# Kernel tuning notes

Measured on AMD Instinct MI355X. Metric: run time of the kernel, lower is better.

The kernel has to match this reference:

```python
import jax, jax.numpy as jnp
import numpy as np

SEQ_LEN = 12      # PRED_LEN
H_DIM = 128
EMB_DIM = 64
NPEDS = 65536


def setup_inputs() -> dict:
    key = jax.random.key(0)
    ks = jax.random.split(key, 12)
    s = 0.05
    return {
        "last_pos": jax.random.normal(ks[0], (NPEDS, 2), jnp.float32),
        "last_pos_rel": jax.random.normal(ks[1], (NPEDS, 2), jnp.float32),
        "h0": jax.random.normal(ks[2], (NPEDS, H_DIM), jnp.float32),
        "c0": jax.random.normal(ks[3], (NPEDS, H_DIM), jnp.float32),
        # LSTM params (torch gate order: i, f, g, o)
        "w_ih": jax.random.normal(ks[4], (4 * H_DIM, EMB_DIM), jnp.float32) * s,
        "w_hh": jax.random.normal(ks[5], (4 * H_DIM, H_DIM), jnp.float32) * s,
        "b_ih": jax.random.normal(ks[6], (4 * H_DIM,), jnp.float32) * s,
        "b_hh": jax.random.normal(ks[7], (4 * H_DIM,), jnp.float32) * s,
        # spatial_embedding: Linear(2, EMB_DIM)
        "w_se": jax.random.normal(ks[8], (EMB_DIM, 2), jnp.float32) * s,
        "b_se": jax.random.normal(ks[9], (EMB_DIM,), jnp.float32) * s,
        # hidden2pos: Linear(H_DIM, 2)
        "w_hp": jax.random.normal(ks[10], (2, H_DIM), jnp.float32) * s,
        "b_hp": jax.random.normal(ks[11], (2,), jnp.float32) * s,
    }


def reference(last_pos, last_pos_rel, h0, c0,
              w_ih, w_hh, b_ih, b_hh, w_se, b_se, w_hp, b_hp):
    b = b_ih + b_hh  # fold the two LSTM biases
    dec_in0 = last_pos_rel @ w_se.T + b_se          # [N, EMB]

    def step(carry, _):
        h, c, dec_in, lp = carry
        gates = dec_in @ w_ih.T + h @ w_hh.T + b    # [N, 4H]
        i, f, g, o = jnp.split(gates, 4, axis=-1)
        c = jax.nn.sigmoid(f) * c + jax.nn.sigmoid(i) * jnp.tanh(g)
        h = jax.nn.sigmoid(o) * jnp.tanh(c)
        rel = h @ w_hp.T + b_hp                     # [N, 2]
        lp = rel + lp                               # curr_pos
        dec_in = rel @ w_se.T + b_se                # next embedding input
        return (h, c, dec_in, lp), rel

    _, rels = jax.lax.scan(step, (h0, c0, dec_in0, last_pos), None, length=SEQ_LEN)
    return rels  # [SEQ_LEN, N, 2] == pred_traj_fake_rel
```

## Files before the change

### kernel.cpp

```cpp
#include <hip/hip_runtime.h>
#include <hip/hip_bf16.h>

typedef __attribute__((ext_vector_type(8))) short bf16x8;
typedef __attribute__((ext_vector_type(4))) short bf16x4;
typedef __attribute__((ext_vector_type(4))) float f32x4;

#define NPEDS 65536
#define SEQ 12
#define HD 128
#define ED 64
#define MBLK 64
#define P1 136
#define WHH_FRAGS 128
#define WEFF_FRAGS 132
#define NFRAGS (WHH_FRAGS + WEFF_FRAGS)
#define L2E 1.44269504088896340736f
#define NEG2L (-2.88539008177792681472f)

__device__ __forceinline__ short f2bf(float x) {
  __hip_bfloat16 b = __float2bfloat16(x);
  return __builtin_bit_cast(short, b);
}
__device__ __forceinline__ float exp2_(float x) {
#if __has_builtin(__builtin_amdgcn_exp2f)
  return __builtin_amdgcn_exp2f(x);
#else
  return exp2f(x);
#endif
}

__device__ __forceinline__ int pe_grp(int a) {
  return (a >> 3) * 32 + (a & 3) * 8 + ((a >> 2) & 1) * 4;
}

__global__ void prep_kernel(const float* __restrict__ w_ih,
                            const float* __restrict__ w_hh,
                            const float* __restrict__ w_se,
                            const float* __restrict__ w_hp,
                            const float* __restrict__ b_ih,
                            const float* __restrict__ b_hh,
                            const float* __restrict__ b_se,
                            const float* __restrict__ b_hp,
                            short* __restrict__ wsB, float* __restrict__ fl) {
  int t = blockIdx.x * 256 + threadIdx.x;
  if (t < WHH_FRAGS * 64) {
    int frag = t >> 6, l = t & 63;
    int cc = frag >> 4, g = (frag >> 2) & 3, kt = frag & 3;
    float fac = (g == 2) ? 2.0f * L2E : L2E;
    int n = g * HD + cc * 16 + (l & 15);
    bf16x8 v;
#pragma unroll
    for (int e = 0; e < 8; ++e) {
      int k = kt * 32 + ((l >> 4) << 2) + (e & 3) + ((e >> 2) << 4);
      v[e] = f2bf(w_hh[n * HD + k] * fac);
    }
    *(bf16x8*)(wsB + (size_t)frag * 512 + l * 8) = v;
  } else if (t < NFRAGS * 64) {
    int u = t - WHH_FRAGS * 64;
    int frag = u >> 6, l = u & 63;
    int llo = l & 15;
    int ks[8];
#pragma unroll
    for (int e = 0; e < 8; ++e)
      ks[e] = (frag & 3) * 32 + ((l >> 4) << 2) + (e & 3) + ((e >> 2) << 4);
    float acc[8];
    if (frag < 128) {
      int cc = frag >> 4, g = (frag >> 2) & 3;
      float fac = (g == 2) ? 2.0f * L2E : L2E;
      int n = g * HD + cc * 16 + llo;
#pragma unroll
      for (int e = 0; e < 8; ++e) acc[e] = w_hh[n * HD + ks[e]];
      for (int j = 0; j < ED; ++j) {
        float wij = w_ih[n * ED + j];
        float se0 = w_se[2 * j], se1 = w_se[2 * j + 1];
#pragma unroll
        for (int e = 0; e < 8; ++e)
          acc[e] += wij * (se0 * w_hp[ks[e]] + se1 * w_hp[HD + ks[e]]);
      }
#pragma unroll
      for (int e = 0; e < 8; ++e) acc[e] *= fac;
    } else {
#pragma unroll
      for (int e = 0; e < 8; ++e)
        acc[e] = (llo < 2) ? w_hp[llo * HD + ks[e]] : 0.f;
    }
    bf16x8 v;
#pragma unroll
    for (int e = 0; e < 8; ++e) v[e] = f2bf(acc[e]);
    *(bf16x8*)(wsB + (size_t)(WHH_FRAGS + frag) * 512 + l * 8) = v;
  } else if (t < NFRAGS * 64 + 512) {
    int n = t - NFRAGS * 64;
    float fac = ((n >> 7) == 2) ? 2.0f * L2E : L2E;
    float b = b_ih[n] + b_hh[n];
    float s0 = 0.f, w20 = 0.f, w21 = 0.f;
    for (int j = 0; j < ED; ++j) {
      float wij = w_ih[n * ED + j];
      s0 += wij * b_se[j];
      w20 += wij * w_se[2 * j];
      w21 += wij * w_se[2 * j + 1];
    }
    fl[n] = fac * (b + s0 + w20 * b_hp[0] + w21 * b_hp[1]);
    fl[512 + n] = fac * (b + s0);
    fl[1024 + 2 * n] = fac * w20;
    fl[1024 + 2 * n + 1] = fac * w21;
  }
}

__global__ __launch_bounds__(512, 4) void lstm_kernel(
    const float* __restrict__ lpr, const float* __restrict__ h0,
    const float* __restrict__ c0, const float* __restrict__ b_hp,
    const short* __restrict__ wsB, const float* __restrict__ fl,
    float* __restrict__ out) {
  __shared__ __align__(16) short hb[2][MBLK * P1];
  __shared__ __align__(16) short s_wsR[4 * 512];
  __shared__ float s_beff[512];
  __shared__ float s_lpr[MBLK * 2];

  const int tid = threadIdx.x;
  const int cc = tid >> 6;
  const int l = tid & 63;
  const int lhi = l >> 4;
  const int llo = l & 15;
  const int p0 = blockIdx.x * MBLK;
  const int hoff = (cc >> 1) * 32 + (llo >> 2) * 8 + (cc & 1) * 4 + (llo & 3);

  if (tid < 128) s_lpr[tid] = lpr[(size_t)p0 * 2 + tid];
  s_beff[tid] = fl[tid];
  ((unsigned long long*)s_wsR)[tid] =
      ((const unsigned long long*)(wsB + (size_t)(WHH_FRAGS + 128) * 512))[tid];

  bf16x8 Bw[4][4];
#pragma unroll
  for (int g = 0; g < 4; ++g)
#pragma unroll
    for (int kt = 0; kt < 4; ++kt)
      Bw[g][kt] = *(const bf16x8*)(wsB +
                      (size_t)((cc * 4 + g) * 4 + kt) * 512 + l * 8);

  float creg[4][4];
#pragma unroll
  for (int Mt = 0; Mt < 4; ++Mt)
#pragma unroll
    for (int r = 0; r < 4; ++r)
      creg[Mt][r] =
          c0[(size_t)(p0 + Mt * 16 + lhi * 4 + r) * HD + cc * 16 + llo];

  const float bhp_l = (llo < 2) ? b_hp[llo] : 0.f;

#pragma unroll
  for (int i = 0; i < 4; ++i) {
    int grp = i * 512 + tid;
    int p = grp >> 5, a = grp & 31;
    f32x4 v = *(const f32x4*)(h0 + (size_t)(p0 + p) * HD + a * 4);
    bf16x4 s;
    s[0] = f2bf(v[0]); s[1] = f2bf(v[1]); s[2] = f2bf(v[2]); s[3] = f2bf(v[3]);
    *(bf16x4*)(&hb[0][p * P1 + pe_grp(a)]) = s;
  }
  __syncthreads();

  auto update_mt = [&](f32x4 (&acc)[4], float (&cr)[4], int rowb, short* An) {
#pragma unroll
    for (int r = 0; r < 4; ++r) {
      float yi = acc[0][r], yf = acc[1][r];
      float yg = acc[2][r], yo = acc[3][r];
      float P = 1.f + exp2_(-yf);
      float Q = 1.f + exp2_(-yi);
      float R = 1.f + exp2_(-yg);
      float QR = Q * R;
      float rD = __builtin_amdgcn_rcpf(P * QR);
      float cn = (cr[r] * QR + (2.f - R) * P) * rD;
      cr[r] = cn;
      float T = 1.f + exp2_(cn * NEG2L);
      float S = 1.f + exp2_(-yo);
      float hn = (2.f - T) * __builtin_amdgcn_rcpf(S * T);
      An[(rowb + r) * P1 + hoff] = f2bf(hn);
    }
  };

  {
    float b0r[4], w20r[4], w21r[4];
#pragma unroll
    for (int g = 0; g < 4; ++g) {
      int n = g * HD + cc * 16 + llo;
      b0r[g] = fl[512 + n];
      w20r[g] = fl[1024 + 2 * n];
      w21r[g] = fl[1024 + 2 * n + 1];
    }
#pragma unroll
    for (int Mt = 0; Mt < 4; ++Mt) {
      bf16x8 Af[4];
#pragma unroll
      for (int kt = 0; kt < 4; ++kt)
        Af[kt] =
            *(const bf16x8*)(&hb[0][(Mt * 16 + llo) * P1 + kt * 32 + lhi * 8]);
      f32x4 acc[4];
#pragma unroll
      for (int g = 0; g < 4; ++g)
#pragma unroll
        for (int r = 0; r < 4; ++r) {
          int row = Mt * 16 + lhi * 4 + r;
          acc[g][r] =
              b0r[g] + w20r[g] * s_lpr[row * 2] + w21r[g] * s_lpr[row * 2 + 1];
        }
#pragma unroll
      for (int kt = 0; kt < 4; ++kt)
#pragma unroll
        for (int g = 0; g < 4; ++g)
          acc[g] = __builtin_amdgcn_mfma_f32_16x16x32_bf16(Af[kt], Bw[g][kt],
                                                           acc[g], 0, 0, 0);
      update_mt(acc, creg[Mt], Mt * 16 + lhi * 4, hb[1]);
    }
    __syncthreads();
  }

  const short* wsW = wsB + (size_t)WHH_FRAGS * 512;
#pragma unroll
  for (int g = 0; g < 4; ++g)
#pragma unroll
    for (int kt = 0; kt < 4; ++kt)
      Bw[g][kt] = *(const bf16x8*)(wsW +
                      (size_t)((cc * 4 + g) * 4 + kt) * 512 + l * 8);

  const int relMt = cc - 4;
  for (int s = 1; s < SEQ; ++s) {
    const short* A = hb[s & 1];
    short* An = hb[(s + 1) & 1];
    f32x4 ar = {bhp_l, bhp_l, bhp_l, bhp_l};
#pragma unroll
    for (int Mt = 0; Mt < 4; ++Mt) {
      bf16x8 Af[4];
#pragma unroll
      for (int kt = 0; kt < 4; ++kt)
        Af[kt] =
            *(const bf16x8*)(&A[(Mt * 16 + llo) * P1 + kt * 32 + lhi * 8]);
      f32x4 acc[4];
#pragma unroll
      for (int g = 0; g < 4; ++g) {
        float b = s_beff[g * HD + cc * 16 + llo];
        acc[g] = {b, b, b, b};
      }
#pragma unroll
      for (int kt = 0; kt < 4; ++kt)
#pragma unroll
        for (int g = 0; g < 4; ++g)
          acc[g] = __builtin_amdgcn_mfma_f32_16x16x32_bf16(Af[kt], Bw[g][kt],
                                                           acc[g], 0, 0, 0);
      if (cc >= 4 && Mt == relMt) {
#pragma unroll
        for (int kt = 0; kt < 4; ++kt) {
          bf16x8 BfR = *(const bf16x8*)(s_wsR + kt * 512 + l * 8);
          ar = __builtin_amdgcn_mfma_f32_16x16x32_bf16(Af[kt], BfR, ar, 0, 0,
                                                       0);
        }
      }
      update_mt(acc, creg[Mt], Mt * 16 + lhi * 4, An);
    }
    if (cc >= 4 && llo < 2) {
#pragma unroll
      for (int r = 0; r < 4; ++r)
        out[(size_t)(s - 1) * (NPEDS * 2) +
            (size_t)(p0 + relMt * 16 + lhi * 4 + r) * 2 + llo] = ar[r];
    }
    __syncthreads();
  }

  if (cc >= 4) {
    const short* A = hb[SEQ & 1];
    f32x4 ar = {bhp_l, bhp_l, bhp_l, bhp_l};
#pragma unroll
    for (int kt = 0; kt < 4; ++kt) {
      bf16x8 BfR = *(const bf16x8*)(s_wsR + kt * 512 + l * 8);
      bf16x8 Afr =
          *(const bf16x8*)(&A[(relMt * 16 + llo) * P1 + kt * 32 + lhi * 8]);
      ar = __builtin_amdgcn_mfma_f32_16x16x32_bf16(Afr, BfR, ar, 0, 0, 0);
    }
    if (llo < 2) {
#pragma unroll
      for (int r = 0; r < 4; ++r)
        out[(size_t)(SEQ - 1) * (NPEDS * 2) +
            (size_t)(p0 + relMt * 16 + lhi * 4 + r) * 2 + llo] = ar[r];
    }
  }
}

extern "C" void kernel_launch(void* const* d_in, const int* in_sizes, int n_in,
                              void* d_out, int out_size, void* d_ws,
                              size_t ws_size, hipStream_t stream) {
  const float* lpr = (const float*)d_in[1];
  const float* h0 = (const float*)d_in[2];
  const float* c0 = (const float*)d_in[3];
  const float* w_ih = (const float*)d_in[4];
  const float* w_hh = (const float*)d_in[5];
  const float* b_ih = (const float*)d_in[6];
  const float* b_hh = (const float*)d_in[7];
  const float* w_se = (const float*)d_in[8];
  const float* b_se = (const float*)d_in[9];
  const float* w_hp = (const float*)d_in[10];
  const float* b_hp = (const float*)d_in[11];
  short* wsB = (short*)d_ws;
  float* fl = (float*)((char*)d_ws + (size_t)NFRAGS * 512 * sizeof(short));
  float* out = (float*)d_out;

  prep_kernel<<<67, 256, 0, stream>>>(w_ih, w_hh, w_se, w_hp, b_ih, b_hh,
                                      b_se, b_hp, wsB, fl);
  lstm_kernel<<<NPEDS / MBLK, 512, 0, stream>>>(lpr, h0, c0, b_hp, wsB, fl,
                                                out);
}
```

Before: 186.8 us.

## Swap MFMA operands so weights are A, double pedestrians per block

Transposes the per-step gate GEMM so the weight fragments are the A operand and the hidden state is B. Each lane now holds 4 consecutive hidden units for one pedestrian, which allows vectorized bf16x4 writes of h into a new swizzled LDS layout. The block tile grows from 64 to 128 pedestrians with 8 pedestrian tiles per wave, and launch bounds drop to 2 blocks per CU. Bias and hidden2pos weights move from LDS into registers. All 8 waves now compute rel outputs instead of 4. The cost is higher register pressure from 8 c-state tiles per thread and lower occupancy, in exchange for amortizing weight fragments across more MFMAs and fewer LDS stores.

```diff
diff --git a/kernel.cpp b/kernel.cpp
--- a/kernel.cpp
+++ b/kernel.cpp
@@ -4,13 +4,14 @@
 typedef __attribute__((ext_vector_type(8))) short bf16x8;
 typedef __attribute__((ext_vector_type(4))) short bf16x4;
 typedef __attribute__((ext_vector_type(4))) float f32x4;
+typedef __attribute__((ext_vector_type(2))) float f32x2;
 
 #define NPEDS 65536
 #define SEQ 12
 #define HD 128
 #define ED 64
-#define MBLK 64
-#define P1 136
+#define MBLK 128
+#define NPT 8
 #define WHH_FRAGS 128
 #define WEFF_FRAGS 132
 #define NFRAGS (WHH_FRAGS + WEFF_FRAGS)
@@ -29,8 +30,8 @@
 #endif
 }
 
-__device__ __forceinline__ int pe_grp(int a) {
-  return (a >> 3) * 32 + (a & 3) * 8 + ((a >> 2) & 1) * 4;
+__device__ __forceinline__ int hoff(int Pt, int cg, int lhi, int llo) {
+  return (((Pt * 8 + cg) * 4 + lhi) * 16 + llo) * 4;
 }
 
 __global__ void prep_kernel(const float* __restrict__ w_ih,
@@ -106,15 +107,12 @@
   }
 }
 
-__global__ __launch_bounds__(512, 4) void lstm_kernel(
+__global__ __launch_bounds__(512, 2) void lstm_kernel(
     const float* __restrict__ lpr, const float* __restrict__ h0,
     const float* __restrict__ c0, const float* __restrict__ b_hp,
     const short* __restrict__ wsB, const float* __restrict__ fl,
     float* __restrict__ out) {
-  __shared__ __align__(16) short hb[2][MBLK * P1];
-  __shared__ __align__(16) short s_wsR[4 * 512];
-  __shared__ float s_beff[512];
-  __shared__ float s_lpr[MBLK * 2];
+  __shared__ short hb[2][NPT * 8 * 4 * 16 * 4];
 
   const int tid = threadIdx.x;
   const int cc = tid >> 6;
@@ -122,43 +120,49 @@
   const int lhi = l >> 4;
   const int llo = l & 15;
   const int p0 = blockIdx.x * MBLK;
-  const int hoff = (cc >> 1) * 32 + (llo >> 2) * 8 + (cc & 1) * 4 + (llo & 3);
-
-  if (tid < 128) s_lpr[tid] = lpr[(size_t)p0 * 2 + tid];
-  s_beff[tid] = fl[tid];
-  ((unsigned long long*)s_wsR)[tid] =
-      ((const unsigned long long*)(wsB + (size_t)(WHH_FRAGS + 128) * 512))[tid];
-
-  bf16x8 Bw[4][4];
+
+  bf16x8 Aw[4][4];
 #pragma unroll
   for (int g = 0; g < 4; ++g)
 #pragma unroll
     for (int kt = 0; kt < 4; ++kt)
-      Bw[g][kt] = *(const bf16x8*)(wsB +
+      Aw[g][kt] = *(const bf16x8*)(wsB +
                       (size_t)((cc * 4 + g) * 4 + kt) * 512 + l * 8);
-
-  float creg[4][4];
-#pragma unroll
-  for (int Mt = 0; Mt < 4; ++Mt)
-#pragma unroll
-    for (int r = 0; r < 4; ++r)
-      creg[Mt][r] =
-          c0[(size_t)(p0 + Mt * 16 + lhi * 4 + r) * HD + cc * 16 + llo];
-
-  const float bhp_l = (llo < 2) ? b_hp[llo] : 0.f;
-
-#pragma unroll
-  for (int i = 0; i < 4; ++i) {
-    int grp = i * 512 + tid;
-    int p = grp >> 5, a = grp & 31;
-    f32x4 v = *(const f32x4*)(h0 + (size_t)(p0 + p) * HD + a * 4);
-    bf16x4 s;
-    s[0] = f2bf(v[0]); s[1] = f2bf(v[1]); s[2] = f2bf(v[2]); s[3] = f2bf(v[3]);
-    *(bf16x4*)(&hb[0][p * P1 + pe_grp(a)]) = s;
+  bf16x8 Whp[4];
+#pragma unroll
+  for (int kt = 0; kt < 4; ++kt)
+    Whp[kt] = *(const bf16x8*)(wsB +
+                  (size_t)(WHH_FRAGS + 128 + kt) * 512 + l * 8);
+
+  f32x4 beffv[4];
+#pragma unroll
+  for (int g = 0; g < 4; ++g)
+    beffv[g] = *(const f32x4*)&fl[g * HD + cc * 16 + lhi * 4];
+
+  float creg[NPT][4];
+#pragma unroll
+  for (int Pt = 0; Pt < NPT; ++Pt) {
+    f32x4 cv = *(const f32x4*)&c0[(size_t)(p0 + Pt * 16 + llo) * HD +
+                                  cc * 16 + lhi * 4];
+#pragma unroll
+    for (int r = 0; r < 4; ++r) creg[Pt][r] = cv[r];
+  }
+  const float bhp0 = b_hp[0], bhp1 = b_hp[1];
+
+#pragma unroll
+  for (int i = 0; i < 8; ++i) {
+    int idx = i * 512 + tid;
+    int a = idx & 31, ped = idx >> 5;
+    f32x4 v = *(const f32x4*)&h0[(size_t)(p0 + ped) * HD + a * 4];
+    bf16x4 sv;
+    sv[0] = f2bf(v[0]); sv[1] = f2bf(v[1]);
+    sv[2] = f2bf(v[2]); sv[3] = f2bf(v[3]);
+    *(bf16x4*)&hb[0][hoff(ped >> 4, a >> 2, a & 3, ped & 15)] = sv;
   }
   __syncthreads();
 
-  auto update_mt = [&](f32x4 (&acc)[4], float (&cr)[4], int rowb, short* An) {
+  auto update_pt = [&](f32x4 (&acc)[4], float (&cr)[4], short* An, int Pt) {
+    bf16x4 hn4;
 #pragma unroll
     for (int r = 0; r < 4; ++r) {
       float yi = acc[0][r], yf = acc[1][r];
@@ -172,43 +176,45 @@
       cr[r] = cn;
       float T = 1.f + exp2_(cn * NEG2L);
       float S = 1.f + exp2_(-yo);
-      float hn = (2.f - T) * __builtin_amdgcn_rcpf(S * T);
-      An[(rowb + r) * P1 + hoff] = f2bf(hn);
-    }
+      hn4[r] = f2bf((2.f - T) * __builtin_amdgcn_rcpf(S * T));
+    }
+    *(bf16x4*)&An[hoff(Pt, cc, lhi, llo)] = hn4;
   };
 
   {
-    float b0r[4], w20r[4], w21r[4];
+    f32x4 b0v[4], wa[4], wb[4];
 #pragma unroll
     for (int g = 0; g < 4; ++g) {
-      int n = g * HD + cc * 16 + llo;
-      b0r[g] = fl[512 + n];
-      w20r[g] = fl[1024 + 2 * n];
-      w21r[g] = fl[1024 + 2 * n + 1];
-    }
-#pragma unroll
-    for (int Mt = 0; Mt < 4; ++Mt) {
-      bf16x8 Af[4];
+      int n0 = g * HD + cc * 16 + lhi * 4;
+      b0v[g] = *(const f32x4*)&fl[512 + n0];
+      wa[g] = *(const f32x4*)&fl[1024 + 2 * n0];
+      wb[g] = *(const f32x4*)&fl[1024 + 2 * n0 + 4];
+    }
+#pragma unroll
+    for (int Pt = 0; Pt < NPT; ++Pt) {
+      f32x2 lp = *(const f32x2*)&lpr[(size_t)(p0 + Pt * 16 + llo) * 2];
+      bf16x8 Bh[4];
+#pragma unroll
+      for (int kt = 0; kt < 4; ++kt) {
+        bf16x4 lo = *(const bf16x4*)&hb[0][hoff(Pt, 2 * kt, lhi, llo)];
+        bf16x4 hi = *(const bf16x4*)&hb[0][hoff(Pt, 2 * kt + 1, lhi, llo)];
+        Bh[kt] = __builtin_shufflevector(lo, hi, 0, 1, 2, 3, 4, 5, 6, 7);
+      }
+      f32x4 acc[4];
+#pragma unroll
+      for (int g = 0; g < 4; ++g) {
+        acc[g][0] = b0v[g][0] + wa[g][0] * lp[0] + wa[g][1] * lp[1];
+        acc[g][1] = b0v[g][1] + wa[g][2] * lp[0] + wa[g][3] * lp[1];
+        acc[g][2] = b0v[g][2] + wb[g][0] * lp[0] + wb[g][1] * lp[1];
+        acc[g][3] = b0v[g][3] + wb[g][2] * lp[0] + wb[g][3] * lp[1];
+      }
 #pragma unroll
       for (int kt = 0; kt < 4; ++kt)
-        Af[kt] =
-            *(const bf16x8*)(&hb[0][(Mt * 16 + llo) * P1 + kt * 32 + lhi * 8]);
-      f32x4 acc[4];
-#pragma unroll
-      for (int g = 0; g < 4; ++g)
-#pragma unroll
-        for (int r = 0; r < 4; ++r) {
-          int row = Mt * 16 + lhi * 4 + r;
-          acc[g][r] =
-              b0r[g] + w20r[g] * s_lpr[row * 2] + w21r[g] * s_lpr[row * 2 + 1];
-        }
-#pragma unroll
-      for (int kt = 0; kt < 4; ++kt)
 #pragma unroll
         for (int g = 0; g < 4; ++g)
-          acc[g] = __builtin_amdgcn_mfma_f32_16x16x32_bf16(Af[kt], Bw[g][kt],
+          acc[g] = __builtin_amdgcn_mfma_f32_16x16x32_bf16(Aw[g][kt], Bh[kt],
                                                            acc[g], 0, 0, 0);
-      update_mt(acc, creg[Mt], Mt * 16 + lhi * 4, hb[1]);
+      update_pt(acc, creg[Pt], hb[1], Pt);
     }
     __syncthreads();
   }
@@ -218,67 +224,61 @@
   for (int g = 0; g < 4; ++g)
 #pragma unroll
     for (int kt = 0; kt < 4; ++kt)
-      Bw[g][kt] = *(const bf16x8*)(wsW +
+      Aw[g][kt] = *(const bf16x8*)(wsW +
                       (size_t)((cc * 4 + g) * 4 + kt) * 512 + l * 8);
 
-  const int relMt = cc - 4;
   for (int s = 1; s < SEQ; ++s) {
     const short* A = hb[s & 1];
     short* An = hb[(s + 1) & 1];
-    f32x4 ar = {bhp_l, bhp_l, bhp_l, bhp_l};
-#pragma unroll
-    for (int Mt = 0; Mt < 4; ++Mt) {
-      bf16x8 Af[4];
+#pragma unroll
+    for (int Pt = 0; Pt < NPT; ++Pt) {
+      bf16x8 Bh[4];
+#pragma unroll
+      for (int kt = 0; kt < 4; ++kt) {
+        bf16x4 lo = *(const bf16x4*)&A[hoff(Pt, 2 * kt, lhi, llo)];
+        bf16x4 hi = *(const bf16x4*)&A[hoff(Pt, 2 * kt + 1, lhi, llo)];
+        Bh[kt] = __builtin_shufflevector(lo, hi, 0, 1, 2, 3, 4, 5, 6, 7);
+      }
+      f32x4 acc[4];
+#pragma unroll
+      for (int g = 0; g < 4; ++g) acc[g] = beffv[g];
 #pragma unroll
       for (int kt = 0; kt < 4; ++kt)
-        Af[kt] =
-            *(const bf16x8*)(&A[(Mt * 16 + llo) * P1 + kt * 32 + lhi * 8]);
-      f32x4 acc[4];
-#pragma unroll
-      for (int g = 0; g < 4; ++g) {
-        float b = s_beff[g * HD + cc * 16 + llo];
-        acc[g] = {b, b, b, b};
-      }
-#pragma unroll
-      for (int kt = 0; kt < 4; ++kt)
 #pragma unroll
         for (int g = 0; g < 4; ++g)
-          acc[g] = __builtin_amdgcn_mfma_f32_16x16x32_bf16(Af[kt], Bw[g][kt],
+          acc[g] = __builtin_amdgcn_mfma_f32_16x16x32_bf16(Aw[g][kt], Bh[kt],
                                                            acc[g], 0, 0, 0);
-      if (cc >= 4 && Mt == relMt) {
-#pragma unroll
-        for (int kt = 0; kt < 4; ++kt) {
-          bf16x8 BfR = *(const bf16x8*)(s_wsR + kt * 512 + l * 8);
-          ar = __builtin_amdgcn_mfma_f32_16x16x32_bf16(Af[kt], BfR, ar, 0, 0,
-                                                       0);
+      if (Pt == cc) {
+        f32x4 ar = {lhi == 0 ? bhp0 : 0.f, lhi == 0 ? bhp1 : 0.f, 0.f, 0.f};
+#pragma unroll
+        for (int kt = 0; kt < 4; ++kt)
+          ar = __builtin_amdgcn_mfma_f32_16x16x32_bf16(Whp[kt], Bh[kt], ar, 0,
+                                                       0, 0);
+        if (lhi == 0) {
+          f32x2 rv = {ar[0], ar[1]};
+          *(f32x2*)&out[(size_t)(s - 1) * (NPEDS * 2) +
+                        (size_t)(p0 + cc * 16 + llo) * 2] = rv;
         }
       }
-      update_mt(acc, creg[Mt], Mt * 16 + lhi * 4, An);
-    }
-    if (cc >= 4 && llo < 2) {
-#pragma unroll
-      for (int r = 0; r < 4; ++r)
-        out[(size_t)(s - 1) * (NPEDS * 2) +
-            (size_t)(p0 + relMt * 16 + lhi * 4 + r) * 2 + llo] = ar[r];
+      update_pt(acc, creg[Pt], An, Pt);
     }
     __syncthreads();
   }
 
-  if (cc >= 4) {
+  {
     const short* A = hb[SEQ & 1];
-    f32x4 ar = {bhp_l, bhp_l, bhp_l, bhp_l};
+    f32x4 ar = {lhi == 0 ? bhp0 : 0.f, lhi == 0 ? bhp1 : 0.f, 0.f, 0.f};
 #pragma unroll
     for (int kt = 0; kt < 4; ++kt) {
-      bf16x8 BfR = *(const bf16x8*)(s_wsR + kt * 512 + l * 8);
-      bf16x8 Afr =
-          *(const bf16x8*)(&A[(relMt * 16 + llo) * P1 + kt * 32 + lhi * 8]);
-      ar = __builtin_amdgcn_mfma_f32_16x16x32_bf16(Afr, BfR, ar, 0, 0, 0);
-    }
-    if (llo < 2) {
-#pragma unroll
-      for (int r = 0; r < 4; ++r)
-        out[(size_t)(SEQ - 1) * (NPEDS * 2) +
-            (size_t)(p0 + relMt * 16 + lhi * 4 + r) * 2 + llo] = ar[r];
+      bf16x4 lo = *(const bf16x4*)&A[hoff(cc, 2 * kt, lhi, llo)];
+      bf16x4 hi = *(const bf16x4*)&A[hoff(cc, 2 * kt + 1, lhi, llo)];
+      bf16x8 Bh = __builtin_shufflevector(lo, hi, 0, 1, 2, 3, 4, 5, 6, 7);
+      ar = __builtin_amdgcn_mfma_f32_16x16x32_bf16(Whp[kt], Bh, ar, 0, 0, 0);
+    }
+    if (lhi == 0) {
+      f32x2 rv = {ar[0], ar[1]};
+      *(f32x2*)&out[(size_t)(SEQ - 1) * (NPEDS * 2) +
+                    (size_t)(p0 + cc * 16 + llo) * 2] = rv;
     }
   }
 }
```

Result: faster. 159.6 us (-14.6%).

## Halve LSTM block to 4 waves, each handling two gate column groups

Applied to the files above, without the earlier changes.

Cuts the block from 512 to 256 threads, so each wave computes two 16-column hidden slices per row tile and keeps two sets of cell-state registers. Weight fragments are no longer held in registers; they are re-read from global memory through volatile loads at every MFMA, which trades register pressure for extra memory and L2 traffic. The hidden2pos projection is now spread across all four waves instead of only the upper four, and the step loop is no longer unrolled. Launch bounds change to 256 threads with 2 blocks per SIMD.

```diff
diff --git a/kernel.cpp b/kernel.cpp
--- a/kernel.cpp
+++ b/kernel.cpp
@@ -106,7 +106,7 @@
   }
 }
 
-__global__ __launch_bounds__(512, 4) void lstm_kernel(
+__global__ __launch_bounds__(256, 2) void lstm_kernel(
     const float* __restrict__ lpr, const float* __restrict__ h0,
     const float* __restrict__ c0, const float* __restrict__ b_hp,
     const short* __restrict__ wsB, const float* __restrict__ fl,
@@ -117,39 +117,39 @@
   __shared__ float s_lpr[MBLK * 2];
 
   const int tid = threadIdx.x;
-  const int cc = tid >> 6;
+  const int w = tid >> 6;
   const int l = tid & 63;
   const int lhi = l >> 4;
   const int llo = l & 15;
   const int p0 = blockIdx.x * MBLK;
-  const int hoff = (cc >> 1) * 32 + (llo >> 2) * 8 + (cc & 1) * 4 + (llo & 3);
+  const int hof0 = (w >> 1) * 32 + (llo >> 2) * 8 + (w & 1) * 4 + (llo & 3);
+  const int hof1 = hof0 + 64;
 
   if (tid < 128) s_lpr[tid] = lpr[(size_t)p0 * 2 + tid];
   s_beff[tid] = fl[tid];
-  ((unsigned long long*)s_wsR)[tid] =
-      ((const unsigned long long*)(wsB + (size_t)(WHH_FRAGS + 128) * 512))[tid];
-
-  bf16x8 Bw[4][4];
-#pragma unroll
-  for (int g = 0; g < 4; ++g)
-#pragma unroll
-    for (int kt = 0; kt < 4; ++kt)
-      Bw[g][kt] = *(const bf16x8*)(wsB +
-                      (size_t)((cc * 4 + g) * 4 + kt) * 512 + l * 8);
-
-  float creg[4][4];
-#pragma unroll
-  for (int Mt = 0; Mt < 4; ++Mt)
-#pragma unroll
-    for (int r = 0; r < 4; ++r)
-      creg[Mt][r] =
-          c0[(size_t)(p0 + Mt * 16 + lhi * 4 + r) * HD + cc * 16 + llo];
+  s_beff[tid + 256] = fl[tid + 256];
+  {
+    const unsigned long long* src =
+        (const unsigned long long*)(wsB + (size_t)(WHH_FRAGS + 128) * 512);
+    ((unsigned long long*)s_wsR)[tid] = src[tid];
+    ((unsigned long long*)s_wsR)[tid + 256] = src[tid + 256];
+  }
+
+  float creg[2][4][4];
+#pragma unroll
+  for (int cci = 0; cci < 2; ++cci)
+#pragma unroll
+    for (int Mt = 0; Mt < 4; ++Mt)
+#pragma unroll
+      for (int r = 0; r < 4; ++r)
+        creg[cci][Mt][r] = c0[(size_t)(p0 + Mt * 16 + lhi * 4 + r) * HD +
+                              (w + cci * 4) * 16 + llo];
 
   const float bhp_l = (llo < 2) ? b_hp[llo] : 0.f;
 
 #pragma unroll
-  for (int i = 0; i < 4; ++i) {
-    int grp = i * 512 + tid;
+  for (int i = 0; i < 8; ++i) {
+    int grp = i * 256 + tid;
     int p = grp >> 5, a = grp & 31;
     f32x4 v = *(const f32x4*)(h0 + (size_t)(p0 + p) * HD + a * 4);
     bf16x4 s;
@@ -158,7 +158,8 @@
   }
   __syncthreads();
 
-  auto update_mt = [&](f32x4 (&acc)[4], float (&cr)[4], int rowb, short* An) {
+  auto update_mt = [&](f32x4 (&acc)[4], float (&cr)[4], int rowb, short* An,
+                       int hof) {
 #pragma unroll
     for (int r = 0; r < 4; ++r) {
       float yi = acc[0][r], yf = acc[1][r];
@@ -173,113 +174,113 @@
       float T = 1.f + exp2_(cn * NEG2L);
       float S = 1.f + exp2_(-yo);
       float hn = (2.f - T) * __builtin_amdgcn_rcpf(S * T);
-      An[(rowb + r) * P1 + hoff] = f2bf(hn);
+      An[(rowb + r) * P1 + hof] = f2bf(hn);
     }
   };
 
+  auto load_af = [&](bf16x8 (&Af)[4], const short* A, int Mt) {
+#pragma unroll
+    for (int kt = 0; kt < 4; ++kt)
+      Af[kt] = *(const bf16x8*)(&A[(Mt * 16 + llo) * P1 + kt * 32 + lhi * 8]);
+  };
+  auto gates = [&](f32x4 (&acc)[4], bf16x8 (&Af)[4], int cc,
+                   const short* wsrc) {
+#pragma unroll
+    for (int g = 0; g < 4; ++g) {
+      float b = s_beff[g * HD + cc * 16 + llo];
+      acc[g] = {b, b, b, b};
+    }
+#pragma unroll
+    for (int kt = 0; kt < 4; ++kt)
+#pragma unroll
+      for (int g = 0; g < 4; ++g) {
+        bf16x8 Bf = *(volatile const bf16x8*)(wsrc +
+                        (size_t)((cc * 4 + g) * 4 + kt) * 512 + l * 8);
+        acc[g] = __builtin_amdgcn_mfma_f32_16x16x32_bf16(Af[kt], Bf, acc[g],
+                                                         0, 0, 0);
+      }
+  };
+  auto rel_do = [&](bf16x8 (&Af)[4], int sout) {
+    f32x4 ar = {bhp_l, bhp_l, bhp_l, bhp_l};
+#pragma unroll
+    for (int kt = 0; kt < 4; ++kt) {
+      bf16x8 wt = *(volatile const bf16x8*)(s_wsR + kt * 512 + l * 8);
+      ar = __builtin_amdgcn_mfma_f32_16x16x32_bf16(Af[kt], wt, ar, 0, 0, 0);
+    }
+    if (llo < 2) {
+#pragma unroll
+      for (int r = 0; r < 4; ++r)
+        out[(size_t)sout * (NPEDS * 2) +
+            (size_t)(p0 + w * 16 + lhi * 4 + r) * 2 + llo] = ar[r];
+    }
+  };
+
   {
-    float b0r[4], w20r[4], w21r[4];
-#pragma unroll
-    for (int g = 0; g < 4; ++g) {
-      int n = g * HD + cc * 16 + llo;
-      b0r[g] = fl[512 + n];
-      w20r[g] = fl[1024 + 2 * n];
-      w21r[g] = fl[1024 + 2 * n + 1];
-    }
+    float b0r[2][4], w20r[2][4], w21r[2][4];
+#pragma unroll
+    for (int cci = 0; cci < 2; ++cci)
+#pragma unroll
+      for (int g = 0; g < 4; ++g) {
+        int n0 = g * HD + (w + cci * 4) * 16 + llo;
+        b0r[cci][g] = fl[512 + n0];
+        w20r[cci][g] = fl[1024 + 2 * n0];
+        w21r[cci][g] = fl[1024 + 2 * n0 + 1];
+      }
 #pragma unroll
     for (int Mt = 0; Mt < 4; ++Mt) {
       bf16x8 Af[4];
-#pragma unroll
-      for (int kt = 0; kt < 4; ++kt)
-        Af[kt] =
-            *(const bf16x8*)(&hb[0][(Mt * 16 + llo) * P1 + kt * 32 + lhi * 8]);
-      f32x4 acc[4];
-#pragma unroll
-      for (int g = 0; g < 4; ++g)
-#pragma unroll
-        for (int r = 0; r < 4; ++r) {
-          int row = Mt * 16 + lhi * 4 + r;
-          acc[g][r] =
-              b0r[g] + w20r[g] * s_lpr[row * 2] + w21r[g] * s_lpr[row * 2 + 1];
-        }
-#pragma unroll
-      for (int kt = 0; kt < 4; ++kt)
+      load_af(Af, hb[0], Mt);
+#pragma unroll
+      for (int cci = 0; cci < 2; ++cci) {
+        int cc = w + cci * 4;
+        f32x4 acc[4];
 #pragma unroll
         for (int g = 0; g < 4; ++g)
-          acc[g] = __builtin_amdgcn_mfma_f32_16x16x32_bf16(Af[kt], Bw[g][kt],
-                                                           acc[g], 0, 0, 0);
-      update_mt(acc, creg[Mt], Mt * 16 + lhi * 4, hb[1]);
+#pragma unroll
+          for (int r = 0; r < 4; ++r) {
+            int row = Mt * 16 + lhi * 4 + r;
+            acc[g][r] = b0r[cci][g] + w20r[cci][g] * s_lpr[row * 2] +
+                        w21r[cci][g] * s_lpr[row * 2 + 1];
+          }
+#pragma unroll
+        for (int kt = 0; kt < 4; ++kt)
+#pragma unroll
+          for (int g = 0; g < 4; ++g) {
+            bf16x8 Bf = *(volatile const bf16x8*)(wsB +
+                            (size_t)((cc * 4 + g) * 4 + kt) * 512 + l * 8);
+            acc[g] = __builtin_amdgcn_mfma_f32_16x16x32_bf16(Af[kt], Bf,
+                                                             acc[g], 0, 0, 0);
+          }
+        update_mt(acc, creg[cci][Mt], Mt * 16 + lhi * 4, hb[1],
+                  cci ? hof1 : hof0);
+      }
     }
     __syncthreads();
   }
 
   const short* wsW = wsB + (size_t)WHH_FRAGS * 512;
-#pragma unroll
-  for (int g = 0; g < 4; ++g)
-#pragma unroll
-    for (int kt = 0; kt < 4; ++kt)
-      Bw[g][kt] = *(const bf16x8*)(wsW +
-                      (size_t)((cc * 4 + g) * 4 + kt) * 512 + l * 8);
-
-  const int relMt = cc - 4;
+#pragma unroll 1
   for (int s = 1; s < SEQ; ++s) {
     const short* A = hb[s & 1];
     short* An = hb[(s + 1) & 1];
-    f32x4 ar = {bhp_l, bhp_l, bhp_l, bhp_l};
 #pragma unroll
     for (int Mt = 0; Mt < 4; ++Mt) {
       bf16x8 Af[4];
-#pragma unroll
-      for (int kt = 0; kt < 4; ++kt)
-        Af[kt] =
-            *(const bf16x8*)(&A[(Mt * 16 + llo) * P1 + kt * 32 + lhi * 8]);
+      load_af(Af, A, Mt);
       f32x4 acc[4];
-#pragma unroll
-      for (int g = 0; g < 4; ++g) {
-        float b = s_beff[g * HD + cc * 16 + llo];
-        acc[g] = {b, b, b, b};
-      }
-#pragma unroll
-      for (int kt = 0; kt < 4; ++kt)
-#pragma unroll
-        for (int g = 0; g < 4; ++g)
-          acc[g] = __builtin_amdgcn_mfma_f32_16x16x32_bf16(Af[kt], Bw[g][kt],
-                                                           acc[g], 0, 0, 0);
-      if (cc >= 4 && Mt == relMt) {
-#pragma unroll
-        for (int kt = 0; kt < 4; ++kt) {
-          bf16x8 BfR = *(const bf16x8*)(s_wsR + kt * 512 + l * 8);
-          ar = __builtin_amdgcn_mfma_f32_16x16x32_bf16(Af[kt], BfR, ar, 0, 0,
-                                                       0);
-        }
-      }
-      update_mt(acc, creg[Mt], Mt * 16 + lhi * 4, An);
-    }
-    if (cc >= 4 && llo < 2) {
-#pragma unroll
-      for (int r = 0; r < 4; ++r)
-        out[(size_t)(s - 1) * (NPEDS * 2) +
-            (size_t)(p0 + relMt * 16 + lhi * 4 + r) * 2 + llo] = ar[r];
+      gates(acc, Af, w, wsW);
+      if (Mt == w) rel_do(Af, s - 1);
+      update_mt(acc, creg[0][Mt], Mt * 16 + lhi * 4, An, hof0);
+      gates(acc, Af, w + 4, wsW);
+      update_mt(acc, creg[1][Mt], Mt * 16 + lhi * 4, An, hof1);
     }
     __syncthreads();
   }
 
-  if (cc >= 4) {
-    const short* A = hb[SEQ & 1];
-    f32x4 ar = {bhp_l, bhp_l, bhp_l, bhp_l};
-#pragma unroll
-    for (int kt = 0; kt < 4; ++kt) {
-      bf16x8 BfR = *(const bf16x8*)(s_wsR + kt * 512 + l * 8);
-      bf16x8 Afr =
-          *(const bf16x8*)(&A[(relMt * 16 + llo) * P1 + kt * 32 + lhi * 8]);
-      ar = __builtin_amdgcn_mfma_f32_16x16x32_bf16(Afr, BfR, ar, 0, 0, 0);
-    }
-    if (llo < 2) {
-#pragma unroll
-      for (int r = 0; r < 4; ++r)
-        out[(size_t)(SEQ - 1) * (NPEDS * 2) +
-            (size_t)(p0 + relMt * 16 + lhi * 4 + r) * 2 + llo] = ar[r];
-    }
+  {
+    bf16x8 Af[4];
+    load_af(Af, hb[SEQ & 1], w);
+    rel_do(Af, SEQ - 1);
   }
 }
 
@@ -303,6 +304,6 @@
 
   prep_kernel<<<67, 256, 0, stream>>>(w_ih, w_hh, w_se, w_hp, b_ih, b_hh,
                                       b_se, b_hp, wsB, fl);
-  lstm_kernel<<<NPEDS / MBLK, 512, 0, stream>>>(lpr, h0, c0, b_hp, wsB, fl,
+  lstm_kernel<<<NPEDS / MBLK, 256, 0, stream>>>(lpr, h0, c0, b_hp, wsB, fl,
                                                 out);
 }
```

Measured after the change: 404.6 us. +116.6%, slower.
